# Kernel optimization log

Measured on AMD Instinct MI355X. Metric: run time of the kernel, lower is better.

Reference implementation:

```python
import jax, jax.numpy as jnp
import numpy as np

IN_F = 256
OUT_F = 256
ALPHA = 0.2  # LeakyReLU negative slope


def _xavier(key, shape, gain=1.414):
    fan_in, fan_out = shape[0], shape[1]
    limit = gain * np.sqrt(6.0 / (fan_in + fan_out))
    return jax.random.uniform(key, shape, jnp.float32, -limit, limit)


def setup_inputs() -> dict:
    key = jax.random.key(0)
    k1, k2, k3, k4, k5, k6 = jax.random.split(key, 6)
    B, N = 8, 2048
    h = jax.random.normal(k1, (B, N, IN_F), jnp.float32)
    adj = jax.random.randint(k2, (B, N, N), 0, 2, jnp.int32)
    lrgt1 = jax.random.normal(k3, (B, N, OUT_F), jnp.float32)
    W1 = _xavier(k4, (IN_F, IN_F))
    W2 = _xavier(k5, (OUT_F, OUT_F))
    a = _xavier(k6, (2 * IN_F, 1))
    return {"h": h, "adj": adj, "lrgt1": lrgt1, "W1": W1, "W2": W2, "a": a}


def reference(h, adj, lrgt1, W1, W2, a):
    # Wh: [B,N,in], wlrgt: [B,N,out]
    Wh = jnp.matmul(h, W1)
    wlrgt = jnp.matmul(lrgt1, W2)
    # additive attention scores: e[b,i,j] = leaky_relu(Wh_i @ a1 + Wh_j @ a2)
    a1 = a[:IN_F, 0]   # [in]
    a2 = a[IN_F:, 0]   # [in]
    Wh1 = jnp.einsum('bnc,c->bn', Wh, a1)  # [B,N]
    Wh2 = jnp.einsum('bnc,c->bn', Wh, a2)  # [B,N]
    e = jax.nn.leaky_relu(Wh1[:, :, None] + Wh2[:, None, :], ALPHA)  # [B,N,N]
    neg = jnp.float32(-9e15)
    masked = jnp.where(adj > 0, e, neg)
    attention = jax.nn.softmax(masked, axis=2)
    # dropout p=0.0 / eval mode -> identity
    h_prime = jnp.matmul(attention, Wh)      # [B,N,in]
    gt_prime = jnp.matmul(attention, wlrgt)  # [B,N,out]
    return (jax.nn.elu(h_prime), jax.nn.elu(gt_prime))
```

## Files before the change

### kernel.cpp

```cpp
#include <hip/hip_runtime.h>
#include <hip/hip_bf16.h>

#define IN_F 256
#define NN   2048
#define BB   8
#define NEGV (-9.0e15f)

typedef unsigned short u16;
typedef __attribute__((ext_vector_type(8))) short short8x;
typedef __attribute__((ext_vector_type(4))) float float4x;

__device__ __forceinline__ u16 f2b(float f) {
    union { float f; unsigned int u; } x; x.f = f;
    unsigned int r = x.u + 0x7FFFu + ((x.u >> 16) & 1u);
    return (u16)(r >> 16);
}

__device__ __forceinline__ void transp_body(const float* __restrict__ src,
                                            u16* __restrict__ dst,
                                            int R, int C, int tid,
                                            float (*tile)[33])
{
    const int per = (R / 32) * (C / 32);
    const int b  = tid / per;
    const int tt = tid % per;
    const int jt = tt / (C / 32);
    const int ct = tt % (C / 32);
    src += (long)b * R * C;
    dst += (long)b * R * C;

    const int tx = threadIdx.x & 31, ty = threadIdx.x >> 5;
#pragma unroll
    for (int i = 0; i < 4; ++i)
        tile[ty + i * 8][tx] = src[(long)(jt * 32 + ty + i * 8) * C + ct * 32 + tx];
    __syncthreads();
#pragma unroll
    for (int i = 0; i < 4; ++i)
        dst[(long)(ct * 32 + ty + i * 8) * R + jt * 32 + tx] = f2b(tile[tx][ty + i * 8]);
}

__global__ __launch_bounds__(256) void prep(const float* __restrict__ h,
                                            const float* __restrict__ g,
                                            const float* __restrict__ W1,
                                            const float* __restrict__ W2,
                                            const float* __restrict__ a,
                                            u16* __restrict__ HbfT,
                                            u16* __restrict__ GbfT,
                                            u16* __restrict__ W1T,
                                            u16* __restrict__ W2T,
                                            float* __restrict__ v1,
                                            float* __restrict__ v2)
{
    __shared__ float tile[32][33];
    __shared__ float s1[IN_F], s2[IN_F];
    const int bid = blockIdx.x;

    if (bid < 4096) {
        transp_body(h, HbfT, NN, IN_F, bid, tile);
    } else if (bid < 8192) {
        transp_body(g, GbfT, NN, IN_F, bid - 4096, tile);
    } else if (bid < 8256) {
        transp_body(W1, W1T, IN_F, IN_F, bid - 8192, tile);
    } else if (bid < 8320) {
        transp_body(W2, W2T, IN_F, IN_F, bid - 8256, tile);
    } else {
        const int t = threadIdx.x;
        s1[t] = a[t];
        s2[t] = a[IN_F + t];
        __syncthreads();
        float acc1 = 0.f, acc2 = 0.f;
        for (int c = 0; c < IN_F; ++c) {
            float w = W1[t * IN_F + c];
            acc1 += w * s1[c];
            acc2 += w * s2[c];
        }
        v1[t] = acc1;
        v2[t] = acc2;
    }
}

__global__ __launch_bounds__(256) void rowdots(const float* __restrict__ h,
                                               const float* __restrict__ v1,
                                               const float* __restrict__ v2,
                                               float* __restrict__ Wh1,
                                               float* __restrict__ Wh2)
{
    const int wave = threadIdx.x >> 6;
    const int lane = threadIdx.x & 63;
    const long row = (long)blockIdx.x * 4 + wave;
    const int c0 = lane * 4;

    float4 v  = *(const float4*)(h + row * IN_F + c0);
    float4 a1 = *(const float4*)(v1 + c0);
    float4 a2 = *(const float4*)(v2 + c0);

    float s1 = v.x * a1.x + v.y * a1.y + v.z * a1.z + v.w * a1.w;
    float s2 = v.x * a2.x + v.y * a2.y + v.z * a2.z + v.w * a2.w;
#pragma unroll
    for (int off = 32; off; off >>= 1) {
        s1 += __shfl_xor(s1, off, 64);
        s2 += __shfl_xor(s2, off, 64);
    }
    if (lane == 0) { Wh1[row] = s1; Wh2[row] = s2; }
}

#define KSTEP(ksv, BC, BN_, AC, AN_, do_a, jnxt)                              \
    {                                                                         \
        if (do_a) {                                                           \
            _Pragma("unroll") for (int rt = 0; rt < 4; ++rt)                  \
                AN_[rt] = *(const short8x*)&ab[(((ksv) + 1) * 4 + rt) * 512 + lane * 8]; \
        }                                                                     \
        _Pragma("unroll") for (int ct = 0; ct < 4; ++ct)                      \
            BN_[ct] = *(const short8x*)(Bp + ct * 16 * NN + (jnxt));          \
        _Pragma("unroll") for (int rt = 0; rt < 4; ++rt)                      \
            _Pragma("unroll") for (int ct = 0; ct < 4; ++ct)                  \
                acc[rt][ct] = __builtin_amdgcn_mfma_f32_16x16x32_bf16(AC[rt], BC[ct], acc[rt][ct], 0, 0, 0); \
    }

#define CHUNK(KCH, ADJC, W4C, ADJN, W4N)                                      \
    {                                                                         \
        const int j0 = (KCH) * 128;                                           \
        if ((KCH) < 15) {                                                     \
            const int jn0 = j0 + 128 + sg * 16;                               \
            _Pragma("unroll") for (int u = 0; u < 4; ++u) {                   \
                W4N[u]  = *(const float4*)(wh2b + jn0 + u * 4);               \
                ADJN[u] = *(const int4*)(adj + adjR + jn0 + u * 4);           \
            }                                                                 \
        }                                                                     \
        union { short8x v; u16 e[8]; } pk0, pk1;                              \
        _Pragma("unroll") for (int u = 0; u < 4; ++u) {                       \
            const float wv4[4] = {W4C[u].x, W4C[u].y, W4C[u].z, W4C[u].w};    \
            const int   av4[4] = {ADJC[u].x, ADJC[u].y, ADJC[u].z, ADJC[u].w};\
            _Pragma("unroll") for (int c = 0; c < 4; ++c) {                   \
                float x = wh1rr + wv4[c];                                     \
                float e = fmaxf(x, 0.2f * x);                                 \
                float p = __expf(e - mv);                                     \
                p = (av4[c] > 0) ? p : 0.0f;                                  \
                lloc += p;                                                    \
                u16 fv = f2b(p);                                              \
                if (u < 2) pk0.e[u * 4 + c] = fv;                             \
                else       pk1.e[(u - 2) * 4 + c] = fv;                       \
            }                                                                 \
        }                                                                     \
        u16* ab = &Afrag[(KCH) & 1][0];                                       \
        *(short8x*)&ab[wbase0]       = pk0.v;                                 \
        *(short8x*)&ab[wbase0 + 128] = pk1.v;                                 \
        asm volatile("s_waitcnt lgkmcnt(0)\n\ts_barrier" ::: "memory");       \
        _Pragma("unroll") for (int rt = 0; rt < 4; ++rt)                      \
            A0[rt] = *(const short8x*)&ab[rt * 512 + lane * 8];               \
        KSTEP(0, B0, B1, A0, A1, 1, j0 + 1 * 32 + bq8)                        \
        KSTEP(1, B1, B0, A1, A0, 1, j0 + 2 * 32 + bq8)                        \
        KSTEP(2, B0, B1, A0, A1, 1, j0 + 3 * 32 + bq8)                        \
        KSTEP(3, B1, B0, A1, A0, 0, (((KCH) < 15) ? (j0 + 128) : j0) + bq8)   \
    }

__global__ __launch_bounds__(512, 2) void attn_mfma(
    const int* __restrict__ adj,
    const u16* __restrict__ HbfT, const u16* __restrict__ GbfT,
    const float* __restrict__ Wh1, const float* __restrict__ Wh2,
    u16* __restrict__ PH, u16* __restrict__ PG)
{
    const int t = threadIdx.x;
    const int wave = t >> 6, lane = t & 63;
    const int bswz = ((blockIdx.x & 7) << 5) | (blockIdx.x >> 3);
    const int b = bswz >> 5;
    const long gi0 = (long)bswz * 64;

    __shared__ __align__(16) u16 Afrag[2][8192];
    __shared__ float sred[512];
    __shared__ float ssc[65];

    const int rr = t >> 3, sg = t & 7;
    const long adjR = (gi0 + rr) * (long)NN;
    const float* wh2b = Wh2 + (long)b * NN;
    const float wh1rr = Wh1[gi0 + rr];

    {
        float4 w = *(const float4*)(wh2b + t * 4);
        sred[t] = fmaxf(fmaxf(w.x, w.y), fmaxf(w.z, w.w));
    }
    __syncthreads();
    if (t < 64) {
        float v = sred[t * 8];
#pragma unroll
        for (int k = 1; k < 8; ++k) v = fmaxf(v, sred[t * 8 + k]);
#pragma unroll
        for (int off = 32; off; off >>= 1) v = fmaxf(v, __shfl_xor(v, off, 64));
        if (t == 0) ssc[64] = v;
    }
    __syncthreads();
    const float mm = wh1rr + ssc[64];
    const float mv = (mm >= 0.f) ? mm : 0.2f * mm;

    const int wbase0 = ((sg >> 1) * 4 + (rr >> 4)) * 512
                     + ((rr & 15) + 16 * (2 * (sg & 1))) * 8;

    float4x acc[4][4];
#pragma unroll
    for (int rt = 0; rt < 4; ++rt)
#pragma unroll
        for (int ct = 0; ct < 4; ++ct) acc[rt][ct] = (float4x)0.0f;

    const int bn = lane & 15, bq = lane >> 4, bq8 = bq * 8;
    const long hbase = (long)b * IN_F * NN;
    const u16* Bp = ((wave < 4) ? HbfT : GbfT) + hbase
                  + (long)((wave & 3) * 64 + bn) * NN;

    float lloc = 0.f;

    short8x A0[4], A1[4], B0[4], B1[4];
    int4   adjA[4], adjB[4];
    float4 w4A[4], w4B[4];

#pragma unroll
    for (int u = 0; u < 4; ++u) {
        adjA[u] = *(const int4*)(adj + adjR + sg * 16 + u * 4);
        w4A[u]  = *(const float4*)(wh2b + sg * 16 + u * 4);
        adjB[u] = adjA[u];
        w4B[u]  = w4A[u];
    }
#pragma unroll
    for (int ct = 0; ct < 4; ++ct)
        B0[ct] = *(const short8x*)(Bp + ct * 16 * NN + bq8);

    for (int kp = 0; kp < 8; ++kp) {
        CHUNK(kp * 2,     adjA, w4A, adjB, w4B)
        CHUNK(kp * 2 + 1, adjB, w4B, adjA, w4A)
    }

    sred[t] = lloc;
    __syncthreads();
    if (t < 64) {
        float v = sred[t * 8];
#pragma unroll
        for (int k = 1; k < 8; ++k) v += sred[t * 8 + k];
        ssc[t] = 1.0f / v;
    }
    __syncthreads();

    u16* dst = (wave < 4) ? PH : PG;
    const int colb = (wave & 3) * 64;
#pragma unroll
    for (int rt = 0; rt < 4; ++rt)
#pragma unroll
        for (int ct = 0; ct < 4; ++ct) {
            const int c = colb + ct * 16 + bn;
#pragma unroll
            for (int reg = 0; reg < 4; ++reg) {
                const int rl = rt * 16 + bq * 4 + reg;
                const float il = ssc[rl];
                const long row = gi0 + rl;
                dst[row * IN_F + c] = f2b(acc[rt][ct][reg] * il);
            }
        }
}

__global__ __launch_bounds__(256) void epi2(const u16* __restrict__ PH,
                                            const u16* __restrict__ PG,
                                            const u16* __restrict__ W1T,
                                            const u16* __restrict__ W2T,
                                            float* __restrict__ out)
{
    int bid = blockIdx.x;
    const u16* X;
    const u16* WT;
    float* o;
    if (bid < 512) { X = PH; WT = W1T; o = out; }
    else           { X = PG; WT = W2T; o = out + (long)BB * NN * IN_F; bid -= 512; }

    const int t = threadIdx.x;
    const int wave = t >> 6, lane = t & 63;
    const long i0 = (long)bid * 32;

    __shared__ __align__(16) u16 Afrag[8 * 2 * 64 * 8];

    const int m = t >> 3, ks0 = t & 7, rt0 = m >> 4, lm = m & 15;
    const u16* xp = X + (i0 + m) * IN_F + ks0 * 32;
#pragma unroll
    for (int q = 0; q < 4; ++q) {
        short8x v = *(const short8x*)(xp + q * 8);
        *(short8x*)&Afrag[((ks0 * 2 + rt0) * 64 + lm + q * 16) * 8] = v;
    }
    __syncthreads();

    float4x acc[2][4];
#pragma unroll
    for (int rt = 0; rt < 2; ++rt)
#pragma unroll
        for (int ct = 0; ct < 4; ++ct) acc[rt][ct] = (float4x)0.0f;

    const int bn = lane & 15, bq = lane >> 4;
#pragma unroll
    for (int ks = 0; ks < 8; ++ks) {
        short8x A0 = *(const short8x*)&Afrag[((ks * 2 + 0) * 64 + lane) * 8];
        short8x A1 = *(const short8x*)&Afrag[((ks * 2 + 1) * 64 + lane) * 8];
#pragma unroll
        for (int ct = 0; ct < 4; ++ct) {
            const int n = wave * 64 + ct * 16 + bn;
            short8x Bw = *(const short8x*)(WT + n * IN_F + ks * 32 + bq * 8);
            acc[0][ct] = __builtin_amdgcn_mfma_f32_16x16x32_bf16(A0, Bw, acc[0][ct], 0, 0, 0);
            acc[1][ct] = __builtin_amdgcn_mfma_f32_16x16x32_bf16(A1, Bw, acc[1][ct], 0, 0, 0);
        }
    }

#pragma unroll
    for (int rt = 0; rt < 2; ++rt)
#pragma unroll
        for (int ct = 0; ct < 4; ++ct) {
            const int n = wave * 64 + ct * 16 + bn;
#pragma unroll
            for (int reg = 0; reg < 4; ++reg) {
                const long row = i0 + rt * 16 + bq * 4 + reg;
                float v = acc[rt][ct][reg];
                v = (v > 0.f) ? v : (__expf(v) - 1.f);
                o[row * IN_F + n] = v;
            }
        }
}

extern "C" void kernel_launch(void* const* d_in, const int* in_sizes, int n_in,
                              void* d_out, int out_size, void* d_ws, size_t ws_size,
                              hipStream_t stream)
{
    int ih = -1, ig = -1, iadj = -1, iw1 = -1, iw2 = -1, ia = -1;
    for (int i = 0; i < n_in; ++i) {
        int s = in_sizes[i];
        if      (s == BB * NN * NN)   { if (iadj < 0) iadj = i; }
        else if (s == BB * NN * IN_F) { if (ih < 0) ih = i; else if (ig < 0) ig = i; }
        else if (s == IN_F * IN_F)    { if (iw1 < 0) iw1 = i; else if (iw2 < 0) iw2 = i; }
        else if (s == 2 * IN_F)       { if (ia < 0) ia = i; }
    }
    if (ih < 0 || ig < 0 || iadj < 0 || iw1 < 0 || iw2 < 0 || ia < 0) {
        ih = 0; iadj = 1; ig = 2; iw1 = 3; iw2 = 4; ia = 5;
    }
    const float* h     = (const float*)d_in[ih];
    const int*   adj   = (const int*)  d_in[iadj];
    const float* lrgt1 = (const float*)d_in[ig];
    const float* W1    = (const float*)d_in[iw1];
    const float* W2    = (const float*)d_in[iw2];
    const float* a     = (const float*)d_in[ia];
    float* out = (float*)d_out;

    float* ws   = (float*)d_ws;
    float* v1   = ws;
    float* v2   = v1 + IN_F;
    float* Wh1  = v2 + IN_F;
    float* Wh2  = Wh1 + BB * NN;
    u16* W1T  = (u16*)(Wh2 + BB * NN);
    u16* W2T  = W1T + IN_F * IN_F;
    u16* HbfT = W2T + IN_F * IN_F;
    u16* GbfT = HbfT + (long)BB * IN_F * NN;
    u16* PH   = GbfT + (long)BB * IN_F * NN;
    u16* PG   = PH + (long)BB * NN * IN_F;

    const int nrows = BB * NN;

    prep     <<<8321,        256, 0, stream>>>(h, lrgt1, W1, W2, a,
                                               HbfT, GbfT, W1T, W2T, v1, v2);
    rowdots  <<<nrows / 4,   256, 0, stream>>>(h, v1, v2, Wh1, Wh2);
    attn_mfma<<<nrows / 64,  512, 0, stream>>>(adj, HbfT, GbfT, Wh1, Wh2, PH, PG);
    epi2     <<<2 * nrows / 32, 256, 0, stream>>>(PH, PG, W1T, W2T, out);
}
```

Measured before the change: 309.7 us.

## Precompute adjacency bitmask in LDS and software-pipeline P generation with MFMA

Before the main loop, the kernel loads the block's entire adjacency row slice once with coalesced reads and packs it into 64-bit ballot masks in shared memory, so the per-thread int4 adjacency loads disappear from the inner loop. The chunk loop is restructured so the next chunk's probability tile is computed and written to the other LDS buffer while the current chunk's MFMAs run. It also prefetches all four B k-steps one chunk ahead and raises wave priority around MFMA issue. This aims to overlap exp/convert work and global loads with matrix math, at the cost of more registers (four B fragment sets) and an extra 16KB of LDS, which could reduce occupancy.

```diff
diff --git a/kernel.cpp b/kernel.cpp
--- a/kernel.cpp
+++ b/kernel.cpp
@@ -7,6 +7,7 @@
 #define NEGV (-9.0e15f)
 
 typedef unsigned short u16;
+typedef unsigned long long u64;
 typedef __attribute__((ext_vector_type(8))) short short8x;
 typedef __attribute__((ext_vector_type(4))) float float4x;
 
@@ -104,54 +105,68 @@
     if (lane == 0) { Wh1[row] = s1; Wh2[row] = s2; }
 }
 
-#define KSTEP(ksv, BC, BN_, AC, AN_, do_a, jnxt)                              \
+#define AREAD(AR, KS)                                                         \
+    _Pragma("unroll") for (int rt = 0; rt < 4; ++rt)                          \
+        AR[rt] = *(const short8x*)&ab[((KS) * 4 + rt) * 512 + lane * 8];
+
+#define MFMA16(AR, G)                                                         \
+    _Pragma("unroll") for (int rt = 0; rt < 4; ++rt)                          \
+        _Pragma("unroll") for (int ct = 0; ct < 4; ++ct)                      \
+            acc[rt][ct] = __builtin_amdgcn_mfma_f32_16x16x32_bf16(AR[rt], G[ct], acc[rt][ct], 0, 0, 0);
+
+#define BISSUE(G, KN, KS)                                                     \
+    _Pragma("unroll") for (int ct = 0; ct < 4; ++ct)                          \
+        G[ct] = *(const short8x*)(Bp + ct * 16 * NN + ((KN) * 128 + (KS) * 32 + bq8));
+
+#define CHUNK2(KCH, W4C, W4N)                                                 \
     {                                                                         \
-        if (do_a) {                                                           \
-            _Pragma("unroll") for (int rt = 0; rt < 4; ++rt)                  \
-                AN_[rt] = *(const short8x*)&ab[(((ksv) + 1) * 4 + rt) * 512 + lane * 8]; \
-        }                                                                     \
-        _Pragma("unroll") for (int ct = 0; ct < 4; ++ct)                      \
-            BN_[ct] = *(const short8x*)(Bp + ct * 16 * NN + (jnxt));          \
-        _Pragma("unroll") for (int rt = 0; rt < 4; ++rt)                      \
-            _Pragma("unroll") for (int ct = 0; ct < 4; ++ct)                  \
-                acc[rt][ct] = __builtin_amdgcn_mfma_f32_16x16x32_bf16(AC[rt], BC[ct], acc[rt][ct], 0, 0, 0); \
-    }
-
-#define CHUNK(KCH, ADJC, W4C, ADJN, W4N)                                      \
-    {                                                                         \
-        const int j0 = (KCH) * 128;                                           \
+        const u16* ab = &Afrag[(KCH) & 1][0];                                 \
+        u16* abn = &Afrag[((KCH) + 1) & 1][0];                                \
+        AREAD(Aa, 0)                                                          \
         if ((KCH) < 15) {                                                     \
-            const int jn0 = j0 + 128 + sg * 16;                               \
+            const u64 mk = maskL[rr][((KCH) + 1) * 2 + (sg >> 2)];            \
+            const unsigned int bits = (unsigned int)((mk >> ((sg & 3) * 16)) & 0xFFFFull); \
+            union { short8x v; u16 e[8]; } pk0, pk1;                          \
             _Pragma("unroll") for (int u = 0; u < 4; ++u) {                   \
-                W4N[u]  = *(const float4*)(wh2b + jn0 + u * 4);               \
-                ADJN[u] = *(const int4*)(adj + adjR + jn0 + u * 4);           \
+                const float wf[4] = {W4C[u].x, W4C[u].y, W4C[u].z, W4C[u].w}; \
+                _Pragma("unroll") for (int c = 0; c < 4; ++c) {               \
+                    float x = wh1rr + wf[c];                                  \
+                    float ev = fmaxf(x, 0.2f * x);                            \
+                    float p = __expf(ev - mv);                                \
+                    p = ((bits >> (u * 4 + c)) & 1u) ? p : 0.0f;              \
+                    lloc += p;                                                \
+                    u16 fv = f2b(p);                                          \
+                    if (u < 2) pk0.e[u * 4 + c] = fv;                         \
+                    else       pk1.e[(u - 2) * 4 + c] = fv;                   \
+                }                                                             \
+            }                                                                 \
+            *(short8x*)&abn[wbase0]       = pk0.v;                            \
+            *(short8x*)&abn[wbase0 + 128] = pk1.v;                            \
+            if ((KCH) < 14) {                                                 \
+                _Pragma("unroll") for (int u = 0; u < 4; ++u)                 \
+                    W4N[u] = *(const float4*)(wh2b + ((KCH) + 2) * 128 + sg * 16 + u * 4); \
             }                                                                 \
         }                                                                     \
-        union { short8x v; u16 e[8]; } pk0, pk1;                              \
-        _Pragma("unroll") for (int u = 0; u < 4; ++u) {                       \
-            const float wv4[4] = {W4C[u].x, W4C[u].y, W4C[u].z, W4C[u].w};    \
-            const int   av4[4] = {ADJC[u].x, ADJC[u].y, ADJC[u].z, ADJC[u].w};\
-            _Pragma("unroll") for (int c = 0; c < 4; ++c) {                   \
-                float x = wh1rr + wv4[c];                                     \
-                float e = fmaxf(x, 0.2f * x);                                 \
-                float p = __expf(e - mv);                                     \
-                p = (av4[c] > 0) ? p : 0.0f;                                  \
-                lloc += p;                                                    \
-                u16 fv = f2b(p);                                              \
-                if (u < 2) pk0.e[u * 4 + c] = fv;                             \
-                else       pk1.e[(u - 2) * 4 + c] = fv;                       \
-            }                                                                 \
-        }                                                                     \
-        u16* ab = &Afrag[(KCH) & 1][0];                                       \
-        *(short8x*)&ab[wbase0]       = pk0.v;                                 \
-        *(short8x*)&ab[wbase0 + 128] = pk1.v;                                 \
+        AREAD(Ab, 1)                                                          \
+        __builtin_amdgcn_s_setprio(1);                                        \
+        MFMA16(Aa, G0)                                                        \
+        __builtin_amdgcn_s_setprio(0);                                        \
+        if ((KCH) < 15) { BISSUE(G0, (KCH) + 1, 0) }                          \
+        AREAD(Aa, 2)                                                          \
+        __builtin_amdgcn_s_setprio(1);                                        \
+        MFMA16(Ab, G1)                                                        \
+        __builtin_amdgcn_s_setprio(0);                                        \
+        if ((KCH) < 15) { BISSUE(G1, (KCH) + 1, 1) }                          \
+        AREAD(Ab, 3)                                                          \
+        __builtin_amdgcn_s_setprio(1);                                        \
+        MFMA16(Aa, G2)                                                        \
+        __builtin_amdgcn_s_setprio(0);                                        \
+        if ((KCH) < 15) { BISSUE(G2, (KCH) + 1, 2) }                          \
+        __builtin_amdgcn_s_setprio(1);                                        \
+        MFMA16(Ab, G3)                                                        \
+        __builtin_amdgcn_s_setprio(0);                                        \
+        if ((KCH) < 15) { BISSUE(G3, (KCH) + 1, 3) }                          \
         asm volatile("s_waitcnt lgkmcnt(0)\n\ts_barrier" ::: "memory");       \
-        _Pragma("unroll") for (int rt = 0; rt < 4; ++rt)                      \
-            A0[rt] = *(const short8x*)&ab[rt * 512 + lane * 8];               \
-        KSTEP(0, B0, B1, A0, A1, 1, j0 + 1 * 32 + bq8)                        \
-        KSTEP(1, B1, B0, A1, A0, 1, j0 + 2 * 32 + bq8)                        \
-        KSTEP(2, B0, B1, A0, A1, 1, j0 + 3 * 32 + bq8)                        \
-        KSTEP(3, B1, B0, A1, A0, 0, (((KCH) < 15) ? (j0 + 128) : j0) + bq8)   \
     }
 
 __global__ __launch_bounds__(512, 2) void attn_mfma(
@@ -167,11 +182,11 @@
     const long gi0 = (long)bswz * 64;
 
     __shared__ __align__(16) u16 Afrag[2][8192];
+    __shared__ u64 maskL[64][32];
     __shared__ float sred[512];
     __shared__ float ssc[65];
 
     const int rr = t >> 3, sg = t & 7;
-    const long adjR = (gi0 + rr) * (long)NN;
     const float* wh2b = Wh2 + (long)b * NN;
     const float wh1rr = Wh1[gi0 + rr];
 
@@ -191,6 +206,19 @@
     __syncthreads();
     const float mm = wh1rr + ssc[64];
     const float mv = (mm >= 0.f) ? mm : 0.2f * mm;
+
+    {
+        u64* maskW = &maskL[0][0];
+#pragma unroll 8
+        for (int it = 0; it < 256; ++it) {
+            const int w = wave * 256 + it;
+            const int row = w >> 5, seg = w & 31;
+            const int v = adj[(gi0 + row) * (long)NN + seg * 64 + lane];
+            const u64 m = __ballot(v > 0);
+            if (lane == 0) maskW[w] = m;
+        }
+    }
+    __syncthreads();
 
     const int wbase0 = ((sg >> 1) * 4 + (rr >> 4)) * 512
                      + ((rr & 15) + 16 * (2 * (sg & 1))) * 8;
@@ -208,24 +236,46 @@
 
     float lloc = 0.f;
 
-    short8x A0[4], A1[4], B0[4], B1[4];
-    int4   adjA[4], adjB[4];
+    short8x Aa[4], Ab[4];
+    short8x G0[4], G1[4], G2[4], G3[4];
     float4 w4A[4], w4B[4];
 
-#pragma unroll
-    for (int u = 0; u < 4; ++u) {
-        adjA[u] = *(const int4*)(adj + adjR + sg * 16 + u * 4);
-        w4A[u]  = *(const float4*)(wh2b + sg * 16 + u * 4);
-        adjB[u] = adjA[u];
-        w4B[u]  = w4A[u];
-    }
-#pragma unroll
-    for (int ct = 0; ct < 4; ++ct)
-        B0[ct] = *(const short8x*)(Bp + ct * 16 * NN + bq8);
+    {
+        const u64 mk = maskL[rr][sg >> 2];
+        const unsigned int bits = (unsigned int)((mk >> ((sg & 3) * 16)) & 0xFFFFull);
+        union { short8x v; u16 e[8]; } pk0, pk1;
+#pragma unroll
+        for (int u = 0; u < 4; ++u) {
+            const float4 wv = *(const float4*)(wh2b + sg * 16 + u * 4);
+            const float wf[4] = {wv.x, wv.y, wv.z, wv.w};
+#pragma unroll
+            for (int c = 0; c < 4; ++c) {
+                float x = wh1rr + wf[c];
+                float ev = fmaxf(x, 0.2f * x);
+                float p = __expf(ev - mv);
+                p = ((bits >> (u * 4 + c)) & 1u) ? p : 0.0f;
+                lloc += p;
+                u16 fv = f2b(p);
+                if (u < 2) pk0.e[u * 4 + c] = fv;
+                else       pk1.e[(u - 2) * 4 + c] = fv;
+            }
+        }
+        u16* ab0 = &Afrag[0][0];
+        *(short8x*)&ab0[wbase0]       = pk0.v;
+        *(short8x*)&ab0[wbase0 + 128] = pk1.v;
+#pragma unroll
+        for (int u = 0; u < 4; ++u)
+            w4A[u] = *(const float4*)(wh2b + 128 + sg * 16 + u * 4);
+        BISSUE(G0, 0, 0)
+        BISSUE(G1, 0, 1)
+        BISSUE(G2, 0, 2)
+        BISSUE(G3, 0, 3)
+        asm volatile("s_waitcnt lgkmcnt(0)\n\ts_barrier" ::: "memory");
+    }
 
     for (int kp = 0; kp < 8; ++kp) {
-        CHUNK(kp * 2,     adjA, w4A, adjB, w4B)
-        CHUNK(kp * 2 + 1, adjB, w4B, adjA, w4A)
+        CHUNK2(kp * 2,     w4A, w4B)
+        CHUNK2(kp * 2 + 1, w4B, w4A)
     }
 
     sred[t] = lloc;
```

New measurement: 429.0 us. 1.39x slower.

## Deepen software pipeline: prefetch full next chunk of B and adj two chunks ahead

Applied to the files above, without the earlier changes.

Restructures the attention inner loop so that all four k-steps of B fragments for the next 128-column chunk are prefetched into four register sets while the current chunk's MFMAs run. The adjacency and Wh2 loads are now issued two chunks ahead instead of one. The LDS A-fragment reads are double-buffered across k-steps. This is meant to hide global-load latency for B and adj behind more MFMA work, at the cost of higher register pressure under launch_bounds(512,2), which could cause spills.

```diff
diff --git a/kernel.cpp b/kernel.cpp
--- a/kernel.cpp
+++ b/kernel.cpp
@@ -4,7 +4,6 @@
 #define IN_F 256
 #define NN   2048
 #define BB   8
-#define NEGV (-9.0e15f)
 
 typedef unsigned short u16;
 typedef __attribute__((ext_vector_type(8))) short short8x;
@@ -104,38 +103,30 @@
     if (lane == 0) { Wh1[row] = s1; Wh2[row] = s2; }
 }
 
-#define KSTEP(ksv, BC, BN_, AC, AN_, do_a, jnxt)                              \
+#define AREAD(AR, KS)                                                         \
+    _Pragma("unroll") for (int rt = 0; rt < 4; ++rt)                          \
+        AR[rt] = *(const short8x*)&ab[((KS) * 4 + rt) * 512 + lane * 8];
+
+#define MFMA16(AR, G)                                                         \
+    _Pragma("unroll") for (int rt = 0; rt < 4; ++rt)                          \
+        _Pragma("unroll") for (int ct = 0; ct < 4; ++ct)                      \
+            acc[rt][ct] = __builtin_amdgcn_mfma_f32_16x16x32_bf16(AR[rt], G[ct], acc[rt][ct], 0, 0, 0);
+
+#define BISSUE(G, KN, KS)                                                     \
+    _Pragma("unroll") for (int ct = 0; ct < 4; ++ct)                          \
+        G[ct] = *(const short8x*)(Bp + ct * 16 * NN + ((KN) * 128 + (KS) * 32 + bq8));
+
+#define CHUNK3(KCH, ADJ, W4)                                                  \
     {                                                                         \
-        if (do_a) {                                                           \
-            _Pragma("unroll") for (int rt = 0; rt < 4; ++rt)                  \
-                AN_[rt] = *(const short8x*)&ab[(((ksv) + 1) * 4 + rt) * 512 + lane * 8]; \
-        }                                                                     \
-        _Pragma("unroll") for (int ct = 0; ct < 4; ++ct)                      \
-            BN_[ct] = *(const short8x*)(Bp + ct * 16 * NN + (jnxt));          \
-        _Pragma("unroll") for (int rt = 0; rt < 4; ++rt)                      \
-            _Pragma("unroll") for (int ct = 0; ct < 4; ++ct)                  \
-                acc[rt][ct] = __builtin_amdgcn_mfma_f32_16x16x32_bf16(AC[rt], BC[ct], acc[rt][ct], 0, 0, 0); \
-    }
-
-#define CHUNK(KCH, ADJC, W4C, ADJN, W4N)                                      \
-    {                                                                         \
-        const int j0 = (KCH) * 128;                                           \
-        if ((KCH) < 15) {                                                     \
-            const int jn0 = j0 + 128 + sg * 16;                               \
-            _Pragma("unroll") for (int u = 0; u < 4; ++u) {                   \
-                W4N[u]  = *(const float4*)(wh2b + jn0 + u * 4);               \
-                ADJN[u] = *(const int4*)(adj + adjR + jn0 + u * 4);           \
-            }                                                                 \
-        }                                                                     \
         union { short8x v; u16 e[8]; } pk0, pk1;                              \
         _Pragma("unroll") for (int u = 0; u < 4; ++u) {                       \
-            const float wv4[4] = {W4C[u].x, W4C[u].y, W4C[u].z, W4C[u].w};    \
-            const int   av4[4] = {ADJC[u].x, ADJC[u].y, ADJC[u].z, ADJC[u].w};\
+            const float wf[4] = {W4[u].x, W4[u].y, W4[u].z, W4[u].w};         \
+            const int   av[4] = {ADJ[u].x, ADJ[u].y, ADJ[u].z, ADJ[u].w};     \
             _Pragma("unroll") for (int c = 0; c < 4; ++c) {                   \
-                float x = wh1rr + wv4[c];                                     \
-                float e = fmaxf(x, 0.2f * x);                                 \
-                float p = __expf(e - mv);                                     \
-                p = (av4[c] > 0) ? p : 0.0f;                                  \
+                float x = wh1rr + wf[c];                                      \
+                float ev = fmaxf(x, 0.2f * x);                                \
+                float p = __expf(ev - mv);                                    \
+                p = (av[c] > 0) ? p : 0.0f;                                   \
                 lloc += p;                                                    \
                 u16 fv = f2b(p);                                              \
                 if (u < 2) pk0.e[u * 4 + c] = fv;                             \
@@ -146,12 +137,25 @@
         *(short8x*)&ab[wbase0]       = pk0.v;                                 \
         *(short8x*)&ab[wbase0 + 128] = pk1.v;                                 \
         asm volatile("s_waitcnt lgkmcnt(0)\n\ts_barrier" ::: "memory");       \
-        _Pragma("unroll") for (int rt = 0; rt < 4; ++rt)                      \
-            A0[rt] = *(const short8x*)&ab[rt * 512 + lane * 8];               \
-        KSTEP(0, B0, B1, A0, A1, 1, j0 + 1 * 32 + bq8)                        \
-        KSTEP(1, B1, B0, A1, A0, 1, j0 + 2 * 32 + bq8)                        \
-        KSTEP(2, B0, B1, A0, A1, 1, j0 + 3 * 32 + bq8)                        \
-        KSTEP(3, B1, B0, A1, A0, 0, (((KCH) < 15) ? (j0 + 128) : j0) + bq8)   \
+        AREAD(Aa, 0)                                                          \
+        AREAD(Ab, 1)                                                          \
+        MFMA16(Aa, G0)                                                        \
+        if ((KCH) < 15) { BISSUE(G0, (KCH) + 1, 0) }                          \
+        AREAD(Aa, 2)                                                          \
+        MFMA16(Ab, G1)                                                        \
+        if ((KCH) < 15) { BISSUE(G1, (KCH) + 1, 1) }                          \
+        AREAD(Ab, 3)                                                          \
+        MFMA16(Aa, G2)                                                        \
+        if ((KCH) < 15) { BISSUE(G2, (KCH) + 1, 2) }                          \
+        MFMA16(Ab, G3)                                                        \
+        if ((KCH) < 15) { BISSUE(G3, (KCH) + 1, 3) }                          \
+        if ((KCH) < 14) {                                                     \
+            const int jp = ((KCH) + 2) * 128 + sg * 16;                       \
+            _Pragma("unroll") for (int u = 0; u < 4; ++u)                     \
+                W4[u]  = *(const float4*)(wh2b + jp + u * 4);                 \
+            _Pragma("unroll") for (int u = 0; u < 4; ++u)                     \
+                ADJ[u] = *(const int4*)(adj + adjR + jp + u * 4);             \
+        }                                                                     \
     }
 
 __global__ __launch_bounds__(512, 2) void attn_mfma(
@@ -208,24 +212,29 @@
 
     float lloc = 0.f;
 
-    short8x A0[4], A1[4], B0[4], B1[4];
+    short8x Aa[4], Ab[4];
+    short8x G0[4], G1[4], G2[4], G3[4];
     int4   adjA[4], adjB[4];
     float4 w4A[4], w4B[4];
 
 #pragma unroll
     for (int u = 0; u < 4; ++u) {
+        w4A[u]  = *(const float4*)(wh2b + sg * 16 + u * 4);
         adjA[u] = *(const int4*)(adj + adjR + sg * 16 + u * 4);
-        w4A[u]  = *(const float4*)(wh2b + sg * 16 + u * 4);
-        adjB[u] = adjA[u];
-        w4B[u]  = w4A[u];
-    }
-#pragma unroll
-    for (int ct = 0; ct < 4; ++ct)
-        B0[ct] = *(const short8x*)(Bp + ct * 16 * NN + bq8);
+    }
+#pragma unroll
+    for (int u = 0; u < 4; ++u) {
+        w4B[u]  = *(const float4*)(wh2b + 128 + sg * 16 + u * 4);
+        adjB[u] = *(const int4*)(adj + adjR + 128 + sg * 16 + u * 4);
+    }
+    BISSUE(G0, 0, 0)
+    BISSUE(G1, 0, 1)
+    BISSUE(G2, 0, 2)
+    BISSUE(G3, 0, 3)
 
     for (int kp = 0; kp < 8; ++kp) {
-        CHUNK(kp * 2,     adjA, w4A, adjB, w4B)
-        CHUNK(kp * 2 + 1, adjB, w4B, adjA, w4A)
+        CHUNK3(kp * 2,     adjA, w4A)
+        CHUNK3(kp * 2 + 1, adjB, w4B)
     }
 
     sred[t] = lloc;
```

Result: slower. 345.4 us (+11.5%).

## Split attention blocks per output matrix and stage Wh2 row in LDS

Applied to the files above, without the earlier changes.

The attention kernel now launches twice as many 256-thread blocks. Each block handles one output matrix (H or G) for a 64-row tile, where before one 512-thread block produced both. Each thread now builds 32 probabilities per chunk instead of 16, and the Wh2 scores are loaded once into shared memory instead of being streamed from global memory per chunk. The cost is that the exp/softmax numerator work and the adjacency reads are duplicated across the two matrix blocks. Fewer threads per block also means more registers per thread for the wider adjacency buffers.

```diff
diff --git a/kernel.cpp b/kernel.cpp
--- a/kernel.cpp
+++ b/kernel.cpp
@@ -4,7 +4,6 @@
 #define IN_F 256
 #define NN   2048
 #define BB   8
-#define NEGV (-9.0e15f)
 
 typedef unsigned short u16;
 typedef __attribute__((ext_vector_type(8))) short short8x;
@@ -117,34 +116,37 @@
                 acc[rt][ct] = __builtin_amdgcn_mfma_f32_16x16x32_bf16(AC[rt], BC[ct], acc[rt][ct], 0, 0, 0); \
     }
 
-#define CHUNK(KCH, ADJC, W4C, ADJN, W4N)                                      \
+#define CHUNK7(KCH, ADJC, ADJN)                                               \
     {                                                                         \
         const int j0 = (KCH) * 128;                                           \
-        if ((KCH) < 15) {                                                     \
-            const int jn0 = j0 + 128 + sg * 16;                               \
-            _Pragma("unroll") for (int u = 0; u < 4; ++u) {                   \
-                W4N[u]  = *(const float4*)(wh2b + jn0 + u * 4);               \
-                ADJN[u] = *(const int4*)(adj + adjR + jn0 + u * 4);           \
+        union { short8x v; u16 e[8]; } pk0, pk1, pk2, pk3;                    \
+        _Pragma("unroll") for (int u = 0; u < 8; ++u) {                       \
+            const float4 wv = *(const float4*)&wh2L[j0 + sg * 32 + u * 4];    \
+            const float wf[4] = {wv.x, wv.y, wv.z, wv.w};                     \
+            const int   av[4] = {ADJC[u].x, ADJC[u].y, ADJC[u].z, ADJC[u].w}; \
+            _Pragma("unroll") for (int c = 0; c < 4; ++c) {                   \
+                float x = wh1rr + wf[c];                                      \
+                float ev = fmaxf(x, 0.2f * x);                                \
+                float p = __expf(ev - mv);                                    \
+                p = (av[c] > 0) ? p : 0.0f;                                   \
+                lloc += p;                                                    \
+                u16 fv = f2b(p);                                              \
+                if (u < 2)      pk0.e[(u & 1) * 4 + c] = fv;                  \
+                else if (u < 4) pk1.e[(u & 1) * 4 + c] = fv;                  \
+                else if (u < 6) pk2.e[(u & 1) * 4 + c] = fv;                  \
+                else            pk3.e[(u & 1) * 4 + c] = fv;                  \
             }                                                                 \
         }                                                                     \
-        union { short8x v; u16 e[8]; } pk0, pk1;                              \
-        _Pragma("unroll") for (int u = 0; u < 4; ++u) {                       \
-            const float wv4[4] = {W4C[u].x, W4C[u].y, W4C[u].z, W4C[u].w};    \
-            const int   av4[4] = {ADJC[u].x, ADJC[u].y, ADJC[u].z, ADJC[u].w};\
-            _Pragma("unroll") for (int c = 0; c < 4; ++c) {                   \
-                float x = wh1rr + wv4[c];                                     \
-                float e = fmaxf(x, 0.2f * x);                                 \
-                float p = __expf(e - mv);                                     \
-                p = (av4[c] > 0) ? p : 0.0f;                                  \
-                lloc += p;                                                    \
-                u16 fv = f2b(p);                                              \
-                if (u < 2) pk0.e[u * 4 + c] = fv;                             \
-                else       pk1.e[(u - 2) * 4 + c] = fv;                       \
-            }                                                                 \
+        if ((KCH) < 15) {                                                     \
+            const long o = adjR + ((KCH) + 1) * 128 + sg * 32;                \
+            _Pragma("unroll") for (int u = 0; u < 8; ++u)                     \
+                ADJN[u] = *(const int4*)(adj + o + u * 4);                    \
         }                                                                     \
         u16* ab = &Afrag[(KCH) & 1][0];                                       \
         *(short8x*)&ab[wbase0]       = pk0.v;                                 \
         *(short8x*)&ab[wbase0 + 128] = pk1.v;                                 \
+        *(short8x*)&ab[wbase0 + 256] = pk2.v;                                 \
+        *(short8x*)&ab[wbase0 + 384] = pk3.v;                                 \
         asm volatile("s_waitcnt lgkmcnt(0)\n\ts_barrier" ::: "memory");       \
         _Pragma("unroll") for (int rt = 0; rt < 4; ++rt)                      \
             A0[rt] = *(const short8x*)&ab[rt * 512 + lane * 8];               \
@@ -154,7 +156,7 @@
         KSTEP(3, B1, B0, A1, A0, 0, (((KCH) < 15) ? (j0 + 128) : j0) + bq8)   \
     }
 
-__global__ __launch_bounds__(512, 2) void attn_mfma(
+__global__ __launch_bounds__(256, 2) void attn_mfma(
     const int* __restrict__ adj,
     const u16* __restrict__ HbfT, const u16* __restrict__ GbfT,
     const float* __restrict__ Wh1, const float* __restrict__ Wh2,
@@ -162,28 +164,35 @@
 {
     const int t = threadIdx.x;
     const int wave = t >> 6, lane = t & 63;
-    const int bswz = ((blockIdx.x & 7) << 5) | (blockIdx.x >> 3);
-    const int b = bswz >> 5;
-    const long gi0 = (long)bswz * 64;
+    const int b   = blockIdx.x & 7;
+    const int idx = blockIdx.x >> 3;
+    const int mat = idx & 1;
+    const int rbl = idx >> 1;
+    const long gi0 = ((long)b * 32 + rbl) * 64;
 
     __shared__ __align__(16) u16 Afrag[2][8192];
-    __shared__ float sred[512];
+    __shared__ float wh2L[2048];
+    __shared__ float sred[256];
     __shared__ float ssc[65];
 
-    const int rr = t >> 3, sg = t & 7;
+    const int rr = t >> 2, sg = t & 3;
     const long adjR = (gi0 + rr) * (long)NN;
     const float* wh2b = Wh2 + (long)b * NN;
     const float wh1rr = Wh1[gi0 + rr];
 
     {
-        float4 w = *(const float4*)(wh2b + t * 4);
-        sred[t] = fmaxf(fmaxf(w.x, w.y), fmaxf(w.z, w.w));
+        float4 w0 = *(const float4*)(wh2b + t * 8);
+        float4 w1 = *(const float4*)(wh2b + t * 8 + 4);
+        *(float4*)&wh2L[t * 8]     = w0;
+        *(float4*)&wh2L[t * 8 + 4] = w1;
+        float m = fmaxf(fmaxf(fmaxf(w0.x, w0.y), fmaxf(w0.z, w0.w)),
+                        fmaxf(fmaxf(w1.x, w1.y), fmaxf(w1.z, w1.w)));
+        sred[t] = m;
     }
     __syncthreads();
     if (t < 64) {
-        float v = sred[t * 8];
-#pragma unroll
-        for (int k = 1; k < 8; ++k) v = fmaxf(v, sred[t * 8 + k]);
+        float v = fmaxf(fmaxf(sred[t * 4], sred[t * 4 + 1]),
+                        fmaxf(sred[t * 4 + 2], sred[t * 4 + 3]));
 #pragma unroll
         for (int off = 32; off; off >>= 1) v = fmaxf(v, __shfl_xor(v, off, 64));
         if (t == 0) ssc[64] = v;
@@ -192,8 +201,7 @@
     const float mm = wh1rr + ssc[64];
     const float mv = (mm >= 0.f) ? mm : 0.2f * mm;
 
-    const int wbase0 = ((sg >> 1) * 4 + (rr >> 4)) * 512
-                     + ((rr & 15) + 16 * (2 * (sg & 1))) * 8;
+    const int wbase0 = (sg * 4 + (rr >> 4)) * 512 + (rr & 15) * 8;
 
     float4x acc[4][4];
 #pragma unroll
@@ -202,44 +210,39 @@
         for (int ct = 0; ct < 4; ++ct) acc[rt][ct] = (float4x)0.0f;
 
     const int bn = lane & 15, bq = lane >> 4, bq8 = bq * 8;
-    const long hbase = (long)b * IN_F * NN;
-    const u16* Bp = ((wave < 4) ? HbfT : GbfT) + hbase
-                  + (long)((wave & 3) * 64 + bn) * NN;
+    const u16* Bp = (mat ? GbfT : HbfT) + (long)b * IN_F * NN
+                  + (long)(wave * 64 + bn) * NN;
 
     float lloc = 0.f;
 
     short8x A0[4], A1[4], B0[4], B1[4];
-    int4   adjA[4], adjB[4];
-    float4 w4A[4], w4B[4];
-
-#pragma unroll
-    for (int u = 0; u < 4; ++u) {
-        adjA[u] = *(const int4*)(adj + adjR + sg * 16 + u * 4);
-        w4A[u]  = *(const float4*)(wh2b + sg * 16 + u * 4);
-        adjB[u] = adjA[u];
-        w4B[u]  = w4A[u];
-    }
+    int4 adjA[8], adjB[8];
+
+#pragma unroll
+    for (int u = 0; u < 8; ++u)
+        adjA[u] = *(const int4*)(adj + adjR + sg * 32 + u * 4);
+#pragma unroll
+    for (int u = 0; u < 8; ++u)
+        adjB[u] = *(const int4*)(adj + adjR + 128 + sg * 32 + u * 4);
 #pragma unroll
     for (int ct = 0; ct < 4; ++ct)
         B0[ct] = *(const short8x*)(Bp + ct * 16 * NN + bq8);
 
     for (int kp = 0; kp < 8; ++kp) {
-        CHUNK(kp * 2,     adjA, w4A, adjB, w4B)
-        CHUNK(kp * 2 + 1, adjB, w4B, adjA, w4A)
+        CHUNK7(kp * 2,     adjA, adjB)
+        CHUNK7(kp * 2 + 1, adjB, adjA)
     }
 
     sred[t] = lloc;
     __syncthreads();
     if (t < 64) {
-        float v = sred[t * 8];
-#pragma unroll
-        for (int k = 1; k < 8; ++k) v += sred[t * 8 + k];
+        float v = sred[t * 4] + sred[t * 4 + 1] + sred[t * 4 + 2] + sred[t * 4 + 3];
         ssc[t] = 1.0f / v;
     }
     __syncthreads();
 
-    u16* dst = (wave < 4) ? PH : PG;
-    const int colb = (wave & 3) * 64;
+    u16* dst = mat ? PG : PH;
+    const int colb = wave * 64;
 #pragma unroll
     for (int rt = 0; rt < 4; ++rt)
 #pragma unroll
@@ -358,6 +361,6 @@
     prep     <<<8321,        256, 0, stream>>>(h, lrgt1, W1, W2, a,
                                                HbfT, GbfT, W1T, W2T, v1, v2);
     rowdots  <<<nrows / 4,   256, 0, stream>>>(h, v1, v2, Wh1, Wh2);
-    attn_mfma<<<nrows / 64,  512, 0, stream>>>(adj, HbfT, GbfT, Wh1, Wh2, PH, PG);
+    attn_mfma<<<nrows / 32,  256, 0, stream>>>(adj, HbfT, GbfT, Wh1, Wh2, PH, PG);
     epi2     <<<2 * nrows / 32, 256, 0, stream>>>(PH, PG, W1T, W2T, out);
 }
```

After: 324.1 us. 1.05x slower.
